# Kernel tuning notes

Measured on AMD Instinct MI355X. Metric: run time of the kernel, lower is better.

## Reference

```python
import jax, jax.numpy as jnp
import numpy as np

N = 32768      # nodes
E = 262144     # edges (avg degree 8)
F = 64         # channels per irrep
Z = 10         # species
R = 8          # radial basis size
H = 64         # radial MLP hidden
P_TP = 5       # TP paths: 0x0->0, 0x1->1, 1x0->1, 1x1->0, 1x1->1
P_SC = 9       # symmetric-contraction paths up to correlation 3
EPS = 0.25     # epsilon ~ 1/sqrt(avg_num_neighbors)


def _split(x):
    # [N, 4F] -> scalars [N,F], vectors [N,F,3] (irreps F x (0e + 1o))
    return x[:, :F], x[:, F:].reshape(x.shape[0], F, 3)


def _merge(s, v):
    return jnp.concatenate([s, v.reshape(v.shape[0], 3 * F)], axis=-1)


def _lin(s, v, Ws, Wv):
    # irreps-wise linear (separate channel mixing per l), fan-in normalized
    inv = 1.0 / np.sqrt(F)
    return (s @ Ws) * inv, jnp.einsum('nfc,fg->ngc', v, Wv) * inv


def _linZ(s, v, Ws, Wv, species):
    # per-species indexed linear, extra 1/sqrt(num_species) as in linZ
    inv = 1.0 / np.sqrt(F * Z)
    return (jnp.einsum('nf,nfg->ng', s, Ws[species]) * inv,
            jnp.einsum('nfc,nfg->ngc', v, Wv[species]) * inv)


def setup_inputs() -> dict:
    key = jax.random.key(0)
    ks = jax.random.split(key, 24)
    f32 = jnp.float32
    return {
        'vectors': jax.random.normal(ks[0], (E, 3), f32),
        'node_feats': jax.random.normal(ks[1], (N, 4 * F), f32),
        'radial_embeddings': jax.random.normal(ks[2], (E, R), f32),
        'W_skip_s': jax.random.normal(ks[3], (Z, F, F), f32),
        'W_skip_v': jax.random.normal(ks[4], (Z, F, F), f32),
        'W_up_s': jax.random.normal(ks[5], (F, F), f32),
        'W_up_v': jax.random.normal(ks[6], (F, F), f32),
        'W_mlp1': jax.random.normal(ks[7], (R, H), f32),
        'W_mlp2': jax.random.normal(ks[8], (H, H), f32),
        'W_mlp3': jax.random.normal(ks[9], (H, H), f32),
        'W_mlp4': jax.random.normal(ks[10], (H, P_TP * F), f32),
        'W_down_s': jax.random.normal(ks[11], (F, F), f32),
        'W_down_v': jax.random.normal(ks[12], (F, F), f32),
        'W_sc': jax.random.normal(ks[13], (Z, P_SC, F), f32),
        'W_post_s': jax.random.normal(ks[14], (F, F), f32),
        'W_post_v': jax.random.normal(ks[15], (F, F), f32),
        'W_out': jax.random.normal(ks[16], (F, 1), f32),
        'node_species': jax.random.randint(ks[17], (N,), 0, Z),
        'senders': jax.random.randint(ks[18], (E,), 0, N),
        'receivers': jax.random.randint(ks[19], (E,), 0, N),
    }


def reference(vectors, node_feats, radial_embeddings, W_skip_s, W_skip_v,
              W_up_s, W_up_v, W_mlp1, W_mlp2, W_mlp3, W_mlp4,
              W_down_s, W_down_v, W_sc, W_post_s, W_post_v, W_out,
              node_species, senders, receivers):
    s, v = _split(node_feats)

    # self connection: per-species skip linear (linZ_skip_tp)
    skip_s, skip_v = _linZ(s, v, W_skip_s, W_skip_v, node_species)

    # linear_up
    s, v = _lin(s, v, W_up_s, W_up_v)

    # spherical harmonics of edge vectors (l=0 is constant, l=1 = unit vector)
    Y1 = vectors / (jnp.linalg.norm(vectors, axis=-1, keepdims=True) + 1e-9)  # [E,3]

    # radial MLP (64,64,64,P_TP*F), no bias, fan-in normalized, silu
    act = jax.nn.silu
    h = act(radial_embeddings @ W_mlp1 * (1.0 / np.sqrt(R)))
    h = act(h @ W_mlp2 * (1.0 / np.sqrt(H)))
    h = act(h @ W_mlp3 * (1.0 / np.sqrt(H)))
    w = (h @ W_mlp4 * (1.0 / np.sqrt(H))).reshape(E, P_TP, F)  # per-edge path weights

    # channelwise tensor product: gather senders, CG-couple with Y, scatter to receivers
    ss = s[senders]              # [E,F]
    vv = v[senders]              # [E,F,3]
    dot = jnp.einsum('efc,ec->ef', vv, Y1)        # 1x1 -> 0
    cross = jnp.cross(vv, Y1[:, None, :])         # 1x1 -> 1
    m_s = w[:, 0] * ss + w[:, 3] * dot
    m_v = (w[:, 1][..., None] * Y1[:, None, :]
           + w[:, 2][..., None] * vv
           + w[:, 4][..., None] * cross * (1.0 / np.sqrt(2.0)))
    s = jax.ops.segment_sum(m_s * EPS, receivers, num_segments=N)  # [N,F]
    v = jax.ops.segment_sum(m_v * EPS, receivers, num_segments=N)  # [N,F,3]

    # linear_down
    s, v = _lin(s, v, W_down_s, W_down_v)

    # per-species symmetric contraction, correlation orders 1..3
    wz = W_sc[node_species]             # [N,P_SC,F]
    vn2 = jnp.sum(v * v, axis=-1)       # [N,F] invariant |v|^2
    s_out = (wz[:, 0] * s + wz[:, 1] * s * s + wz[:, 2] * vn2
             + wz[:, 3] * s ** 3 + wz[:, 4] * s * vn2)
    v_out = (wz[:, 5] + wz[:, 6] * s + wz[:, 7] * s * s + wz[:, 8] * vn2)[..., None] * v

    # linear_post_sc + skip connection
    s, v = _lin(s_out, v_out, W_post_s, W_post_v)
    s = s + skip_s
    v = v + skip_v

    # linear_readout to scalar output irreps (0e)
    node_outputs = s @ W_out * (1.0 / np.sqrt(F))  # [N,1]
    return node_outputs, _merge(s, v)
```

## Files before the change

kernel.cpp:

```cpp
#include <hip/hip_runtime.h>
#include <math.h>


#define NN 32768
#define EE 262144
#define EC 131072
#define ZZ 10
#define NB 128
#define NT_MAX 2064
#define INV8 0.125f
#define INV_SQRT8 0.35355339059327373f
#define INVZ 0.039528470752104741f
#define EPS_C 0.25f
#define RS2 0.70710678118654752f

typedef _Float16 f16;
typedef f16 f16x8 __attribute__((ext_vector_type(8)));
typedef f16 f16x4 __attribute__((ext_vector_type(4)));
typedef float f32x4 __attribute__((ext_vector_type(4)));

#define LDFRAG(fid) (*(const f16x8*)(fragw + ((size_t)(fid) << 9) + (lane << 3)))

__device__ __forceinline__ unsigned bfpair(float lo, float hi) {
  unsigned ul = __float_as_uint(lo);
  unsigned uh = __float_as_uint(hi);
  ul = (ul + 0x7FFFu + ((ul >> 16) & 1u)) >> 16;
  uh = (uh + 0x7FFFu + ((uh >> 16) & 1u)) >> 16;
  return ul | (uh << 16);
}

__device__ __forceinline__ unsigned short f2h(float x) {
  union { f16 h; unsigned short u; } cv;
  cv.h = (f16)x;
  return cv.u;
}

__device__ __forceinline__ f16x8 pack8(float4 a, float4 b) {
  f16x8 r;
  r[0] = (f16)a.x; r[1] = (f16)a.y; r[2] = (f16)a.z; r[3] = (f16)a.w;
  r[4] = (f16)b.x; r[5] = (f16)b.y; r[6] = (f16)b.z; r[7] = (f16)b.w;
  return r;
}

__device__ __forceinline__ float silu_f(float x) {
  return x / (1.0f + __expf(-x));
}

__global__ __launch_bounds__(256) void k_frag(
    const float* __restrict__ W1, const float* __restrict__ W2,
    const float* __restrict__ W3, const float* __restrict__ W4,
    const float* __restrict__ Wdns, const float* __restrict__ Wdnv,
    const float* __restrict__ Wpss, const float* __restrict__ Wpsv,
    const float* __restrict__ Wsks, const float* __restrict__ Wskv,
    const float* __restrict__ Wups, const float* __restrict__ Wupv,
    unsigned short* __restrict__ fragw) {
  int id = blockIdx.x * 256 + threadIdx.x;
  if (id >= 268 * 64) return;
  int fid = id >> 6, lane = id & 63;
  int q = lane >> 4, c = lane & 15;
  const float* W; int K = 64, N = 64, t, ks; float sc; int w4 = 0;
  if (fid < 4)       { W = W1; K = 8; N = 64; t = fid; ks = 0; sc = INV_SQRT8; }
  else if (fid < 12) { W = W2; t = (fid - 4) >> 1;  ks = (fid - 4) & 1;  sc = INV8; }
  else if (fid < 20) { W = W3; t = (fid - 12) >> 1; ks = (fid - 12) & 1; sc = INV8; }
  else if (fid < 60) { W = W4; N = 320; t = (fid - 20) >> 1; ks = (fid - 20) & 1; sc = INV8; w4 = 1; }
  else {
    int f2 = fid - 60; sc = INV8;
    if (f2 < 8)        { W = Wdns; }
    else if (f2 < 16)  { W = Wdnv; f2 -= 8; }
    else if (f2 < 24)  { W = Wpss; f2 -= 16; }
    else if (f2 < 32)  { W = Wpsv; f2 -= 24; }
    else if (f2 < 112) { f2 -= 32; W = Wsks + (f2 >> 3) * 4096; f2 &= 7; sc = INVZ; }
    else if (f2 < 192) { f2 -= 112; W = Wskv + (f2 >> 3) * 4096; f2 &= 7; sc = INVZ; }
    else if (f2 < 200) { W = Wups; f2 -= 192; }
    else               { W = Wupv; f2 -= 200; }
    t = f2 >> 1; ks = f2 & 1;
  }
  int col = w4 ? ((t % 5) * 64 + 4 * c + (t / 5)) : (t * 16 + c);
  unsigned short o[8];
#pragma unroll
  for (int i = 0; i < 8; ++i) {
    int k = ks * 32 + 8 * q + i;
    float v = (k < K) ? W[k * N + col] * sc : 0.0f;
    o[i] = f2h(v);
  }
  *(uint4*)(fragw + (size_t)id * 8) = *(const uint4*)o;
}

__global__ __launch_bounds__(256) void k_hist(const int* __restrict__ rcv,
                                              int* __restrict__ cnt) {
  int e = blockIdx.x * 256 + threadIdx.x;
  atomicAdd(&cnt[rcv[e]], 1);
}

__global__ __launch_bounds__(1024) void k_scan(const int* __restrict__ cnt,
                                               int* __restrict__ row_start,
                                               int* __restrict__ cursor) {
  __shared__ int tot[1024];
  int t = threadIdx.x;
  int base = t * 32;
  int local[32];
  int s = 0;
#pragma unroll
  for (int i = 0; i < 32; ++i) { local[i] = s; s += cnt[base + i]; }
  tot[t] = s;
  __syncthreads();
  for (int off = 1; off < 1024; off <<= 1) {
    int v = (t >= off) ? tot[t - off] : 0;
    __syncthreads();
    tot[t] += v;
    __syncthreads();
  }
  int prefix = (t == 0) ? 0 : tot[t - 1];
#pragma unroll
  for (int i = 0; i < 32; ++i) {
    int v = prefix + local[i];
    row_start[base + i] = v;
    cursor[base + i] = v;
  }
  if (t == 1023) row_start[NN] = prefix + s;
}

__global__ __launch_bounds__(256) void k_fill(const int* __restrict__ rcv,
                                              int* __restrict__ cursor,
                                              int* __restrict__ elist) {
  int e = blockIdx.x * 256 + threadIdx.x;
  int pos = atomicAdd(&cursor[rcv[e]], 1);
  elist[pos] = e;
}

__global__ __launch_bounds__(256) void k_nhist(const int* __restrict__ species,
                                               int* __restrict__ sbins,
                                               int* __restrict__ bcnt) {
  __shared__ int h[ZZ];
  int t = threadIdx.x;
  if (t < ZZ) h[t] = 0;
  __syncthreads();
  int n = blockIdx.x * 256 + t;
  atomicAdd(&h[species[n]], 1);
  __syncthreads();
  if (t < ZZ) {
    bcnt[blockIdx.x * ZZ + t] = h[t];
    atomicAdd(&sbins[32 + t], h[t]);
  }
}

__global__ __launch_bounds__(256) void k_nscan(int* __restrict__ sbins,
                                               const int* __restrict__ bcnt,
                                               int* __restrict__ bbase,
                                               int* __restrict__ tspec) {
  __shared__ int sb[12];
  int t = threadIdx.x;
  if (t == 0) {
    int off = 0;
    for (int z = 0; z < ZZ; ++z) {
      sb[z] = off;
      off += ((sbins[32 + z] + 15) >> 4) << 4;
    }
    sb[ZZ] = off;
  }
  __syncthreads();
  if (t < ZZ) {
    int run = sb[t];
    for (int b = 0; b < NB; ++b) {
      bbase[b * ZZ + t] = run;
      run += bcnt[b * ZZ + t];
    }
  }
  for (int i = t; i < NT_MAX; i += 256) {
    int base = i * 16, z = -1;
#pragma unroll
    for (int zz = 0; zz < ZZ; ++zz)
      if (base >= sb[zz] && base < sb[zz + 1]) z = zz;
    tspec[i] = z;
  }
}

__global__ __launch_bounds__(256) void k_nfill(const int* __restrict__ species,
                                               const int* __restrict__ bbase,
                                               int* __restrict__ nperm) {
  __shared__ int cur[ZZ];
  int t = threadIdx.x;
  if (t < ZZ) cur[t] = bbase[blockIdx.x * ZZ + t];
  __syncthreads();
  int n = blockIdx.x * 256 + t;
  int pos = atomicAdd(&cur[species[n]], 1);
  nperm[pos] = n;
}

__global__ __launch_bounds__(256) void k_up2(
    const float* __restrict__ nf,
    const unsigned short* __restrict__ fragw,
    unsigned short* __restrict__ s_up, unsigned short* __restrict__ v_up) {
  int lane = threadIdx.x & 63;
  int wv = threadIdx.x >> 6;
  int n0 = (blockIdx.x * 4 + wv) * 16;
  int q = lane >> 4, c = lane & 15;
  const f32x4 zero4 = {0.f, 0.f, 0.f, 0.f};
  const float* nrow = nf + (size_t)(n0 + c) * 256;

  f16x8 aS[2], aX[2], aY[2], aZ[2];
#pragma unroll
  for (int ks = 0; ks < 2; ++ks) {
    int k0 = ks * 32 + 8 * q;
    aS[ks] = pack8(*(const float4*)(nrow + k0), *(const float4*)(nrow + k0 + 4));
    float vb[24];
    const float4* vp = (const float4*)(nrow + 64 + 3 * k0);
#pragma unroll
    for (int j = 0; j < 6; ++j) *(float4*)(vb + 4 * j) = vp[j];
#pragma unroll
    for (int i = 0; i < 8; ++i) {
      aX[ks][i] = (f16)vb[3 * i];
      aY[ks][i] = (f16)vb[3 * i + 1];
      aZ[ks][i] = (f16)vb[3 * i + 2];
    }
  }

  f32x4 os[4], ox[4], oy[4], oz[4];
#pragma unroll
  for (int t = 0; t < 4; ++t)
#pragma unroll
    for (int ks = 0; ks < 2; ++ks) {
      f16x8 bS = LDFRAG(252 + t * 2 + ks);
      f16x8 bV = LDFRAG(260 + t * 2 + ks);
      os[t] = __builtin_amdgcn_mfma_f32_16x16x32_f16(aS[ks], bS, ks ? os[t] : zero4, 0, 0, 0);
      ox[t] = __builtin_amdgcn_mfma_f32_16x16x32_f16(aX[ks], bV, ks ? ox[t] : zero4, 0, 0, 0);
      oy[t] = __builtin_amdgcn_mfma_f32_16x16x32_f16(aY[ks], bV, ks ? oy[t] : zero4, 0, 0, 0);
      oz[t] = __builtin_amdgcn_mfma_f32_16x16x32_f16(aZ[ks], bV, ks ? oz[t] : zero4, 0, 0, 0);
    }

#pragma unroll
  for (int t = 0; t < 4; ++t)
#pragma unroll
    for (int r = 0; r < 4; ++r) {
      int n = n0 + 4 * q + r;
      int ch = 16 * t + c;
      s_up[n * 64 + ch] = f2h(os[t][r]);
      v_up[(n * 3 + 0) * 64 + ch] = f2h(ox[t][r]);
      v_up[(n * 3 + 1) * 64 + ch] = f2h(oy[t][r]);
      v_up[(n * 3 + 2) * 64 + ch] = f2h(oz[t][r]);
    }
}

__global__ __launch_bounds__(256) void k_mlp(
    const float* __restrict__ re, const int* __restrict__ elist,
    const float* __restrict__ vecs, const int* __restrict__ snd,
    const unsigned short* __restrict__ fragw,
    const unsigned short* __restrict__ s_up,
    const unsigned short* __restrict__ v_up,
    unsigned short* __restrict__ wm, int ip0) {
  __shared__ float hs[4][2][1088];
  int lane = threadIdx.x & 63;
  int wv = threadIdx.x >> 6;
  int q = lane >> 4, c = lane & 15;
  int ipb = ip0 + (blockIdx.x * 4 + wv) * 32;
  float* hw0 = hs[wv][0];
  float* hw1 = hs[wv][1];
  const f32x4 zero4 = {0.f, 0.f, 0.f, 0.f};

  f16x8 a1[2];
#pragma unroll
  for (int m = 0; m < 2; ++m) {
    f16x8 v = {0, 0, 0, 0, 0, 0, 0, 0};
    if (q == 0) {
      int e = elist[ipb + m * 16 + c];
      const float4* rp = (const float4*)(re + (size_t)e * 8);
      v = pack8(rp[0], rp[1]);
    }
    a1[m] = v;
  }
  {
    f32x4 acc[2][4];
#pragma unroll
    for (int t = 0; t < 4; ++t) {
      f16x8 b = LDFRAG(t);
#pragma unroll
      for (int m = 0; m < 2; ++m)
        acc[m][t] = __builtin_amdgcn_mfma_f32_16x16x32_f16(a1[m], b, zero4, 0, 0, 0);
    }
#pragma unroll
    for (int m = 0; m < 2; ++m) {
      float* hw = (m == 0) ? hw0 : hw1;
#pragma unroll
      for (int t = 0; t < 4; ++t)
#pragma unroll
        for (int r = 0; r < 4; ++r) {
          float x = silu_f(acc[m][t][r]);
          hw[(4 * q + r) * 68 + ((16 * t + c) ^ (r << 3))] = x;
        }
    }
  }

#pragma unroll
  for (int L = 0; L < 2; ++L) {
    int base = 4 + 8 * L;
    f16x8 af[2][2];
#pragma unroll
    for (int m = 0; m < 2; ++m) {
      const float* hw = (m == 0) ? hw0 : hw1;
#pragma unroll
      for (int ks = 0; ks < 2; ++ks) {
        const float* hp = hw + c * 68 + ks * 32 + 8 * (q ^ (c & 3));
        af[m][ks] = pack8(*(const float4*)hp, *(const float4*)(hp + 4));
      }
    }
    f32x4 acc[2][4];
#pragma unroll
    for (int t = 0; t < 4; ++t)
#pragma unroll
      for (int ks = 0; ks < 2; ++ks) {
        f16x8 b = LDFRAG(base + t * 2 + ks);
#pragma unroll
        for (int m = 0; m < 2; ++m)
          acc[m][t] = __builtin_amdgcn_mfma_f32_16x16x32_f16(
              af[m][ks], b, ks ? acc[m][t] : zero4, 0, 0, 0);
      }
#pragma unroll
    for (int m = 0; m < 2; ++m) {
      float* hw = (m == 0) ? hw0 : hw1;
#pragma unroll
      for (int t = 0; t < 4; ++t)
#pragma unroll
        for (int r = 0; r < 4; ++r) {
          float x = silu_f(acc[m][t][r]);
          hw[(4 * q + r) * 68 + ((16 * t + c) ^ (r << 3))] = x;
        }
    }
  }

  size_t orow = (size_t)(ipb - ip0);
#pragma unroll 1
  for (int m = 0; m < 2; ++m) {
    const float* hw = (m == 0) ? hw0 : hw1;
    f16x8 a4k0, a4k1;
    {
      const float* hp0 = hw + c * 68 + 8 * (q ^ (c & 3));
      const float* hp1 = hp0 + 32;
      a4k0 = pack8(*(const float4*)hp0, *(const float4*)(hp0 + 4));
      a4k1 = pack8(*(const float4*)hp1, *(const float4*)(hp1 + 4));
    }

    float Yx[4], Yy[4], Yz[4];
    f16x4 fs[4], fx[4], fy[4], fz[4];
#pragma unroll
    for (int r = 0; r < 4; ++r) {
      int e = elist[ipb + m * 16 + 4 * q + r];
      float ex = vecs[(size_t)e * 3 + 0];
      float ey = vecs[(size_t)e * 3 + 1];
      float ez = vecs[(size_t)e * 3 + 2];
      float rn = 1.0f / (sqrtf(ex * ex + ey * ey + ez * ez) + 1e-9f);
      Yx[r] = ex * rn; Yy[r] = ey * rn; Yz[r] = ez * rn;
      int se = snd[e];
      const unsigned short* sr = s_up + (size_t)se * 64 + 4 * c;
      const unsigned short* vr = v_up + (size_t)se * 192 + 4 * c;
      fs[r] = *(const f16x4*)sr;
      fx[r] = *(const f16x4*)vr;
      fy[r] = *(const f16x4*)(vr + 64);
      fz[r] = *(const f16x4*)(vr + 128);
    }

    float pms[4], pmx[4], pmy[4], pmz[4];
    unsigned k0s[4], k0x[4], k0y[4], k0z[4];
#pragma unroll
    for (int ig = 0; ig < 4; ++ig) {
      f32x4 o[5];
#pragma unroll
      for (int p = 0; p < 5; ++p) {
        f16x8 b0 = LDFRAG(20 + (ig * 5 + p) * 2 + 0);
        f16x8 b1 = LDFRAG(20 + (ig * 5 + p) * 2 + 1);
        o[p] = __builtin_amdgcn_mfma_f32_16x16x32_f16(a4k0, b0, zero4, 0, 0, 0);
        o[p] = __builtin_amdgcn_mfma_f32_16x16x32_f16(a4k1, b1, o[p], 0, 0, 0);
      }
#pragma unroll
      for (int r = 0; r < 4; ++r) {
        float ss = (float)fs[r][ig];
        float vx = (float)fx[r][ig], vy = (float)fy[r][ig], vz = (float)fz[r][ig];
        float dt = vx * Yx[r] + vy * Yy[r] + vz * Yz[r];
        float cx = vy * Yz[r] - vz * Yy[r];
        float cy = vz * Yx[r] - vx * Yz[r];
        float cz = vx * Yy[r] - vy * Yx[r];
        float ms = EPS_C * (o[0][r] * ss + o[3][r] * dt);
        float mx = EPS_C * (o[1][r] * Yx[r] + o[2][r] * vx + o[4][r] * (cx * RS2));
        float my = EPS_C * (o[1][r] * Yy[r] + o[2][r] * vy + o[4][r] * (cy * RS2));
        float mz = EPS_C * (o[1][r] * Yz[r] + o[2][r] * vz + o[4][r] * (cz * RS2));
        if (ig == 0) {
          pms[r] = ms; pmx[r] = mx; pmy[r] = my; pmz[r] = mz;
        } else if (ig == 1) {
          k0s[r] = bfpair(pms[r], ms); k0x[r] = bfpair(pmx[r], mx);
          k0y[r] = bfpair(pmy[r], my); k0z[r] = bfpair(pmz[r], mz);
        } else if (ig == 2) {
          pms[r] = ms; pmx[r] = mx; pmy[r] = my; pmz[r] = mz;
        } else {
          unsigned short* wr = wm + (orow + m * 16 + 4 * q + r) * 256 + 4 * c;
          uint2 v;
          v.x = k0s[r]; v.y = bfpair(pms[r], ms);
          *(uint2*)(wr) = v;
          v.x = k0x[r]; v.y = bfpair(pmx[r], mx);
          *(uint2*)(wr + 64) = v;
          v.x = k0y[r]; v.y = bfpair(pmy[r], my);
          *(uint2*)(wr + 128) = v;
          v.x = k0z[r]; v.y = bfpair(pmz[r], mz);
          *(uint2*)(wr + 192) = v;
        }
      }
    }
  }
}

__global__ __launch_bounds__(256) void k_gather(
    const unsigned short* __restrict__ m_buf,
    const int* __restrict__ row_start,
    float* __restrict__ acc, int e0, int e1) {
  int g = threadIdx.x & 63;
  int wv = threadIdx.x >> 6;
  int n = blockIdx.x * 4 + wv;
  int beg = row_start[n], end = row_start[n + 1];
  int lo = beg > e0 ? beg : e0;
  int hi = end < e1 ? end : e1;
  if (lo >= hi) return;
  float4 a = make_float4(0.f, 0.f, 0.f, 0.f);
  for (int i = lo; i < hi; ++i) {
    uint2 m = *(const uint2*)(m_buf + (size_t)(i - e0) * 256 + g * 4);
    a.x += __uint_as_float(m.x << 16);
    a.y += __uint_as_float(m.x & 0xFFFF0000u);
    a.z += __uint_as_float(m.y << 16);
    a.w += __uint_as_float(m.y & 0xFFFF0000u);
  }
  float* dst = acc + (size_t)n * 256 + g * 4;
  float4 p = *(const float4*)dst;
  *(float4*)dst = make_float4(a.x + p.x, a.y + p.y, a.z + p.z, a.w + p.w);
}

__global__ __launch_bounds__(128) void k_post2(
    const float* __restrict__ nf, const float* __restrict__ acc,
    const unsigned short* __restrict__ fragw,
    const float* __restrict__ Wsc, const float* __restrict__ Wout,
    const int* __restrict__ nperm, const int* __restrict__ tspec,
    float* __restrict__ out) {
  __shared__ float hs[2][2][1088];
  int lane = threadIdx.x & 63;
  int wv = threadIdx.x >> 6;
  int tt = blockIdx.x * 2 + wv;
  int spec = tspec[tt];
  if (spec < 0) return;
  int q = lane >> 4, c = lane & 15;
  float* hw0 = hs[wv][0];
  float* hw1 = hs[wv][1];
  const f32x4 zero4 = {0.f, 0.f, 0.f, 0.f};

  int nA = nperm[tt * 16 + c];
  size_t rowA = (size_t)((nA < 0) ? 0 : nA);
  const float* arow = acc + rowA * 256;
  const float* nrow = nf + rowA * 256;

  f16x8 aS[2], aVX[2], aVY[2], aVZ[2];
  f16x8 kS[2], kX[2], kY[2], kZ[2];
#pragma unroll
  for (int ks = 0; ks < 2; ++ks) {
    int k0 = ks * 32 + 8 * q;
    aS[ks]  = pack8(*(const float4*)(arow + k0),       *(const float4*)(arow + k0 + 4));
    aVX[ks] = pack8(*(const float4*)(arow + 64 + k0),  *(const float4*)(arow + 68 + k0));
    aVY[ks] = pack8(*(const float4*)(arow + 128 + k0), *(const float4*)(arow + 132 + k0));
    aVZ[ks] = pack8(*(const float4*)(arow + 192 + k0), *(const float4*)(arow + 196 + k0));
    kS[ks]  = pack8(*(const float4*)(nrow + k0),       *(const float4*)(nrow + k0 + 4));
    float vb[24];
    const float4* vp = (const float4*)(nrow + 64 + 3 * k0);
#pragma unroll
    for (int j = 0; j < 6; ++j) *(float4*)(vb + 4 * j) = vp[j];
#pragma unroll
    for (int i = 0; i < 8; ++i) {
      kX[ks][i] = (f16)vb[3 * i];
      kY[ks][i] = (f16)vb[3 * i + 1];
      kZ[ks][i] = (f16)vb[3 * i + 2];
    }
  }

  f32x4 ds[4], dvx[4], dvy[4], dvz[4];
#pragma unroll
  for (int t = 0; t < 4; ++t)
#pragma unroll
    for (int ks = 0; ks < 2; ++ks) {
      f16x8 bS = LDFRAG(60 + t * 2 + ks);
      f16x8 bV = LDFRAG(68 + t * 2 + ks);
      ds[t]  = __builtin_amdgcn_mfma_f32_16x16x32_f16(aS[ks],  bS, ks ? ds[t]  : zero4, 0, 0, 0);
      dvx[t] = __builtin_amdgcn_mfma_f32_16x16x32_f16(aVX[ks], bV, ks ? dvx[t] : zero4, 0, 0, 0);
      dvy[t] = __builtin_amdgcn_mfma_f32_16x16x32_f16(aVY[ks], bV, ks ? dvy[t] : zero4, 0, 0, 0);
      dvz[t] = __builtin_amdgcn_mfma_f32_16x16x32_f16(aVZ[ks], bV, ks ? dvz[t] : zero4, 0, 0, 0);
    }

  f32x4 ps[4], pvx[4], pvy[4], pvz[4];
#pragma unroll
  for (int t = 0; t < 4; ++t)
#pragma unroll
    for (int ks = 0; ks < 2; ++ks) {
      f16x8 bs = LDFRAG(92 + spec * 8 + t * 2 + ks);
      f16x8 bv = LDFRAG(172 + spec * 8 + t * 2 + ks);
      ps[t]  = __builtin_amdgcn_mfma_f32_16x16x32_f16(kS[ks], bs, ks ? ps[t]  : zero4, 0, 0, 0);
      pvx[t] = __builtin_amdgcn_mfma_f32_16x16x32_f16(kX[ks], bv, ks ? pvx[t] : zero4, 0, 0, 0);
      pvy[t] = __builtin_amdgcn_mfma_f32_16x16x32_f16(kY[ks], bv, ks ? pvy[t] : zero4, 0, 0, 0);
      pvz[t] = __builtin_amdgcn_mfma_f32_16x16x32_f16(kZ[ks], bv, ks ? pvz[t] : zero4, 0, 0, 0);
    }

  f32x4 so[4], vcm[4];
  const float* wzp = Wsc + spec * 576 + c;
#pragma unroll
  for (int t = 0; t < 4; ++t) {
    int col = 16 * t;
    float w0 = wzp[col], w1 = wzp[64 + col], w2 = wzp[128 + col];
    float w3 = wzp[192 + col], w4 = wzp[256 + col];
    float w5 = wzp[320 + col], w6 = wzp[384 + col];
    float w7 = wzp[448 + col], w8 = wzp[512 + col];
#pragma unroll
    for (int r = 0; r < 4; ++r) {
      float s = ds[t][r];
      float vx = dvx[t][r], vy = dvy[t][r], vz = dvz[t][r];
      float vn2 = vx * vx + vy * vy + vz * vz;
      so[t][r]  = w0 * s + w1 * s * s + w2 * vn2 + w3 * s * s * s + w4 * s * vn2;
      vcm[t][r] = w5 + w6 * s + w7 * s * s + w8 * vn2;
    }
  }

#pragma unroll
  for (int t = 0; t < 4; ++t)
#pragma unroll
    for (int r = 0; r < 4; ++r) {
      int ad = (4 * q + r) * 68 + ((16 * t + c) ^ (r << 3));
      hw0[ad] = so[t][r];
      hw1[ad] = vcm[t][r] * dvx[t][r];
    }
  {
    f16x8 aP0[2], aP1[2];
#pragma unroll
    for (int ks = 0; ks < 2; ++ks) {
      const float* hp0 = hw0 + c * 68 + ks * 32 + 8 * (q ^ (c & 3));
      const float* hp1 = hw1 + c * 68 + ks * 32 + 8 * (q ^ (c & 3));
      aP0[ks] = pack8(*(const float4*)hp0, *(const float4*)(hp0 + 4));
      aP1[ks] = pack8(*(const float4*)hp1, *(const float4*)(hp1 + 4));
    }
#pragma unroll
    for (int t = 0; t < 4; ++t)
#pragma unroll
      for (int ks = 0; ks < 2; ++ks) {
        ps[t]  = __builtin_amdgcn_mfma_f32_16x16x32_f16(aP0[ks], LDFRAG(76 + t * 2 + ks), ps[t], 0, 0, 0);
        pvx[t] = __builtin_amdgcn_mfma_f32_16x16x32_f16(aP1[ks], LDFRAG(84 + t * 2 + ks), pvx[t], 0, 0, 0);
      }
  }
#pragma unroll
  for (int t = 0; t < 4; ++t)
#pragma unroll
    for (int r = 0; r < 4; ++r) {
      int ad = (4 * q + r) * 68 + ((16 * t + c) ^ (r << 3));
      hw0[ad] = vcm[t][r] * dvy[t][r];
      hw1[ad] = vcm[t][r] * dvz[t][r];
    }
  {
    f16x8 aP0[2], aP1[2];
#pragma unroll
    for (int ks = 0; ks < 2; ++ks) {
      const float* hp0 = hw0 + c * 68 + ks * 32 + 8 * (q ^ (c & 3));
      const float* hp1 = hw1 + c * 68 + ks * 32 + 8 * (q ^ (c & 3));
      aP0[ks] = pack8(*(const float4*)hp0, *(const float4*)(hp0 + 4));
      aP1[ks] = pack8(*(const float4*)hp1, *(const float4*)(hp1 + 4));
    }
#pragma unroll
    for (int t = 0; t < 4; ++t)
#pragma unroll
      for (int ks = 0; ks < 2; ++ks) {
        pvy[t] = __builtin_amdgcn_mfma_f32_16x16x32_f16(aP0[ks], LDFRAG(84 + t * 2 + ks), pvy[t], 0, 0, 0);
        pvz[t] = __builtin_amdgcn_mfma_f32_16x16x32_f16(aP1[ks], LDFRAG(84 + t * 2 + ks), pvz[t], 0, 0, 0);
      }
  }

  float wo[4];
#pragma unroll
  for (int t = 0; t < 4; ++t) wo[t] = Wout[16 * t + c];
  int nst[4];
#pragma unroll
  for (int r = 0; r < 4; ++r) nst[r] = nperm[tt * 16 + 4 * q + r];
#pragma unroll
  for (int r = 0; r < 4; ++r) {
    float part = 0.f;
#pragma unroll
    for (int t = 0; t < 4; ++t) part += ps[t][r] * wo[t];
    part += __shfl_xor(part, 1);
    part += __shfl_xor(part, 2);
    part += __shfl_xor(part, 4);
    part += __shfl_xor(part, 8);
    int n = nst[r];
    if (n >= 0) {
      float* orow = out + NN + (size_t)n * 256;
#pragma unroll
      for (int t = 0; t < 4; ++t) {
        int col = 16 * t + c;
        orow[col] = ps[t][r];
        orow[64 + col * 3 + 0] = pvx[t][r];
        orow[64 + col * 3 + 1] = pvy[t][r];
        orow[64 + col * 3 + 2] = pvz[t][r];
      }
      if (c == 0) out[n] = part * INV8;
    }
  }
}

extern "C" void kernel_launch(void* const* d_in, const int* in_sizes, int n_in,
                              void* d_out, int out_size, void* d_ws, size_t ws_size,
                              hipStream_t stream) {
  (void)in_sizes; (void)n_in; (void)out_size; (void)ws_size;
  const float* vecs = (const float*)d_in[0];
  const float* nf   = (const float*)d_in[1];
  const float* re   = (const float*)d_in[2];
  const float* Wsks = (const float*)d_in[3];
  const float* Wskv = (const float*)d_in[4];
  const float* Wups = (const float*)d_in[5];
  const float* Wupv = (const float*)d_in[6];
  const float* W1   = (const float*)d_in[7];
  const float* W2   = (const float*)d_in[8];
  const float* W3   = (const float*)d_in[9];
  const float* W4   = (const float*)d_in[10];
  const float* Wdns = (const float*)d_in[11];
  const float* Wdnv = (const float*)d_in[12];
  const float* Wsc  = (const float*)d_in[13];
  const float* Wpss = (const float*)d_in[14];
  const float* Wpsv = (const float*)d_in[15];
  const float* Wout = (const float*)d_in[16];
  const int* species = (const int*)d_in[17];
  const int* snd     = (const int*)d_in[18];
  const int* rcv     = (const int*)d_in[19];

  float* ws = (float*)d_ws;
  unsigned short* s_up  = (unsigned short*)ws;
  unsigned short* v_up  = (unsigned short*)(ws + 1048576);
  float* acc   = ws + 4194304;
  unsigned short* fragw = (unsigned short*)(ws + 12582912);
  int* row_st  = (int*)(ws + 12651520);
  int* cursor  = (int*)(ws + 12684352);
  int* elist   = (int*)(ws + 12717120);
  int* nperm   = (int*)(ws + 12979264);
  int* tspec   = (int*)(ws + 13012544);
  int* sbins   = (int*)(ws + 13014848);
  int* bcnt    = (int*)(ws + 13014912);
  int* bbase   = (int*)(ws + 13016192);
  unsigned short* wm = (unsigned short*)(ws + 13017472);

  hipMemsetAsync(cursor, 0, NN * sizeof(int), stream);
  hipMemsetAsync(acc, 0, (size_t)NN * 256 * sizeof(float), stream);
  hipMemsetAsync(sbins, 0, 64 * sizeof(int), stream);
  hipMemsetAsync(nperm, 0xFF, NT_MAX * 16 * sizeof(int), stream);
  k_frag<<<67, 256, 0, stream>>>(W1, W2, W3, W4, Wdns, Wdnv, Wpss, Wpsv,
                                 Wsks, Wskv, Wups, Wupv, fragw);
  k_hist<<<EE / 256, 256, 0, stream>>>(rcv, cursor);
  k_scan<<<1, 1024, 0, stream>>>(cursor, row_st, cursor);
  k_fill<<<EE / 256, 256, 0, stream>>>(rcv, cursor, elist);
  k_nhist<<<NB, 256, 0, stream>>>(species, sbins, bcnt);
  k_nscan<<<1, 256, 0, stream>>>(sbins, bcnt, bbase, tspec);
  k_nfill<<<NB, 256, 0, stream>>>(species, bbase, nperm);
  k_up2<<<512, 256, 0, stream>>>(nf, fragw, s_up, v_up);
  for (int c = 0; c < 2; ++c) {
    k_mlp<<<EC / 128, 256, 0, stream>>>(re, elist, vecs, snd, fragw,
                                        s_up, v_up, wm, c * EC);
    k_gather<<<NN / 4, 256, 0, stream>>>(wm, row_st, acc, c * EC, (c + 1) * EC);
  }
  k_post2<<<NT_MAX / 2, 128, 0, stream>>>(nf, acc, fragw, Wsc, Wout,
                                          nperm, tspec, (float*)d_out);
}
```

Baseline: 408.9 us.

## Halve per-wave edge tile in k_mlp and split gather into two channel passes

Each wave in the edge MLP kernel now handles 16 edges instead of 32. The block count doubles and shared memory per wave halves. The sender-feature gather and message write are split into two passes over channel pairs, which lowers live registers, and launch bounds request 4 blocks per SM for higher occupancy. The cost is less reuse of each weight fragment load across edges, narrower global loads and stores (4-byte instead of 8-byte), and a second pass that repeats the gather addressing.

New measurement: 377.6 us. -7.6%, faster.

```diff
diff --git a/kernel.cpp b/kernel.cpp
--- a/kernel.cpp
+++ b/kernel.cpp
@@ -17,6 +17,7 @@
 typedef _Float16 f16;
 typedef f16 f16x8 __attribute__((ext_vector_type(8)));
 typedef f16 f16x4 __attribute__((ext_vector_type(4)));
+typedef f16 f16x2 __attribute__((ext_vector_type(2)));
 typedef float f32x4 __attribute__((ext_vector_type(4)));
 
 #define LDFRAG(fid) (*(const f16x8*)(fragw + ((size_t)(fid) << 9) + (lane << 3)))
@@ -241,139 +242,114 @@
     }
 }
 
-__global__ __launch_bounds__(256) void k_mlp(
+__global__ __launch_bounds__(256, 4) void k_mlp(
     const float* __restrict__ re, const int* __restrict__ elist,
     const float* __restrict__ vecs, const int* __restrict__ snd,
     const unsigned short* __restrict__ fragw,
     const unsigned short* __restrict__ s_up,
     const unsigned short* __restrict__ v_up,
     unsigned short* __restrict__ wm, int ip0) {
-  __shared__ float hs[4][2][1088];
+  __shared__ float hs[4][1088];
   int lane = threadIdx.x & 63;
   int wv = threadIdx.x >> 6;
   int q = lane >> 4, c = lane & 15;
-  int ipb = ip0 + (blockIdx.x * 4 + wv) * 32;
-  float* hw0 = hs[wv][0];
-  float* hw1 = hs[wv][1];
+  int ipb = ip0 + (blockIdx.x * 4 + wv) * 16;
+  float* hw = hs[wv];
   const f32x4 zero4 = {0.f, 0.f, 0.f, 0.f};
 
-  f16x8 a1[2];
-#pragma unroll
-  for (int m = 0; m < 2; ++m) {
-    f16x8 v = {0, 0, 0, 0, 0, 0, 0, 0};
-    if (q == 0) {
-      int e = elist[ipb + m * 16 + c];
-      const float4* rp = (const float4*)(re + (size_t)e * 8);
-      v = pack8(rp[0], rp[1]);
-    }
-    a1[m] = v;
+  f16x8 a1 = {0, 0, 0, 0, 0, 0, 0, 0};
+  if (q == 0) {
+    int e = elist[ipb + c];
+    const float4* rp = (const float4*)(re + (size_t)e * 8);
+    a1 = pack8(rp[0], rp[1]);
   }
   {
-    f32x4 acc[2][4];
-#pragma unroll
-    for (int t = 0; t < 4; ++t) {
-      f16x8 b = LDFRAG(t);
-#pragma unroll
-      for (int m = 0; m < 2; ++m)
-        acc[m][t] = __builtin_amdgcn_mfma_f32_16x16x32_f16(a1[m], b, zero4, 0, 0, 0);
-    }
-#pragma unroll
-    for (int m = 0; m < 2; ++m) {
-      float* hw = (m == 0) ? hw0 : hw1;
-#pragma unroll
-      for (int t = 0; t < 4; ++t)
-#pragma unroll
-        for (int r = 0; r < 4; ++r) {
-          float x = silu_f(acc[m][t][r]);
-          hw[(4 * q + r) * 68 + ((16 * t + c) ^ (r << 3))] = x;
-        }
-    }
+    f32x4 acc[4];
+#pragma unroll
+    for (int t = 0; t < 4; ++t)
+      acc[t] = __builtin_amdgcn_mfma_f32_16x16x32_f16(a1, LDFRAG(t), zero4, 0, 0, 0);
+#pragma unroll
+    for (int t = 0; t < 4; ++t)
+#pragma unroll
+      for (int r = 0; r < 4; ++r) {
+        float x = silu_f(acc[t][r]);
+        hw[(4 * q + r) * 68 + ((16 * t + c) ^ (r << 3))] = x;
+      }
   }
 
 #pragma unroll
   for (int L = 0; L < 2; ++L) {
     int base = 4 + 8 * L;
-    f16x8 af[2][2];
-#pragma unroll
-    for (int m = 0; m < 2; ++m) {
-      const float* hw = (m == 0) ? hw0 : hw1;
-#pragma unroll
-      for (int ks = 0; ks < 2; ++ks) {
-        const float* hp = hw + c * 68 + ks * 32 + 8 * (q ^ (c & 3));
-        af[m][ks] = pack8(*(const float4*)hp, *(const float4*)(hp + 4));
+    f16x8 af0, af1;
+    {
+      const float* hp = hw + c * 68 + 8 * (q ^ (c & 3));
+      af0 = pack8(*(const float4*)hp, *(const float4*)(hp + 4));
+      af1 = pack8(*(const float4*)(hp + 32), *(const float4*)(hp + 36));
+    }
+    f32x4 acc[4];
+#pragma unroll
+    for (int t = 0; t < 4; ++t) {
+      acc[t] = __builtin_amdgcn_mfma_f32_16x16x32_f16(af0, LDFRAG(base + t * 2), zero4, 0, 0, 0);
+      acc[t] = __builtin_amdgcn_mfma_f32_16x16x32_f16(af1, LDFRAG(base + t * 2 + 1), acc[t], 0, 0, 0);
+    }
+#pragma unroll
+    for (int t = 0; t < 4; ++t)
+#pragma unroll
+      for (int r = 0; r < 4; ++r) {
+        float x = silu_f(acc[t][r]);
+        hw[(4 * q + r) * 68 + ((16 * t + c) ^ (r << 3))] = x;
       }
-    }
-    f32x4 acc[2][4];
-#pragma unroll
-    for (int t = 0; t < 4; ++t)
-#pragma unroll
-      for (int ks = 0; ks < 2; ++ks) {
-        f16x8 b = LDFRAG(base + t * 2 + ks);
-#pragma unroll
-        for (int m = 0; m < 2; ++m)
-          acc[m][t] = __builtin_amdgcn_mfma_f32_16x16x32_f16(
-              af[m][ks], b, ks ? acc[m][t] : zero4, 0, 0, 0);
-      }
-#pragma unroll
-    for (int m = 0; m < 2; ++m) {
-      float* hw = (m == 0) ? hw0 : hw1;
-#pragma unroll
-      for (int t = 0; t < 4; ++t)
-#pragma unroll
-        for (int r = 0; r < 4; ++r) {
-          float x = silu_f(acc[m][t][r]);
-          hw[(4 * q + r) * 68 + ((16 * t + c) ^ (r << 3))] = x;
-        }
-    }
+  }
+
+  f16x8 a4k0, a4k1;
+  {
+    const float* hp = hw + c * 68 + 8 * (q ^ (c & 3));
+    a4k0 = pack8(*(const float4*)hp, *(const float4*)(hp + 4));
+    a4k1 = pack8(*(const float4*)(hp + 32), *(const float4*)(hp + 36));
+  }
+
+  int se_[4];
+  float Yx[4], Yy[4], Yz[4];
+#pragma unroll
+  for (int r = 0; r < 4; ++r) {
+    int e = elist[ipb + 4 * q + r];
+    float ex = vecs[(size_t)e * 3 + 0];
+    float ey = vecs[(size_t)e * 3 + 1];
+    float ez = vecs[(size_t)e * 3 + 2];
+    float rn = 1.0f / (sqrtf(ex * ex + ey * ey + ez * ez) + 1e-9f);
+    Yx[r] = ex * rn; Yy[r] = ey * rn; Yz[r] = ez * rn;
+    se_[r] = snd[e];
   }
 
   size_t orow = (size_t)(ipb - ip0);
 #pragma unroll 1
-  for (int m = 0; m < 2; ++m) {
-    const float* hw = (m == 0) ? hw0 : hw1;
-    f16x8 a4k0, a4k1;
-    {
-      const float* hp0 = hw + c * 68 + 8 * (q ^ (c & 3));
-      const float* hp1 = hp0 + 32;
-      a4k0 = pack8(*(const float4*)hp0, *(const float4*)(hp0 + 4));
-      a4k1 = pack8(*(const float4*)hp1, *(const float4*)(hp1 + 4));
-    }
-
-    float Yx[4], Yy[4], Yz[4];
-    f16x4 fs[4], fx[4], fy[4], fz[4];
+  for (int pg = 0; pg < 2; ++pg) {
+    f16x2 gs[4], gx[4], gy[4], gz[4];
 #pragma unroll
     for (int r = 0; r < 4; ++r) {
-      int e = elist[ipb + m * 16 + 4 * q + r];
-      float ex = vecs[(size_t)e * 3 + 0];
-      float ey = vecs[(size_t)e * 3 + 1];
-      float ez = vecs[(size_t)e * 3 + 2];
-      float rn = 1.0f / (sqrtf(ex * ex + ey * ey + ez * ez) + 1e-9f);
-      Yx[r] = ex * rn; Yy[r] = ey * rn; Yz[r] = ez * rn;
-      int se = snd[e];
-      const unsigned short* sr = s_up + (size_t)se * 64 + 4 * c;
-      const unsigned short* vr = v_up + (size_t)se * 192 + 4 * c;
-      fs[r] = *(const f16x4*)sr;
-      fx[r] = *(const f16x4*)vr;
-      fy[r] = *(const f16x4*)(vr + 64);
-      fz[r] = *(const f16x4*)(vr + 128);
-    }
-
+      const unsigned short* sr = s_up + (size_t)se_[r] * 64 + 4 * c + 2 * pg;
+      const unsigned short* vr = v_up + (size_t)se_[r] * 192 + 4 * c + 2 * pg;
+      gs[r] = *(const f16x2*)sr;
+      gx[r] = *(const f16x2*)vr;
+      gy[r] = *(const f16x2*)(vr + 64);
+      gz[r] = *(const f16x2*)(vr + 128);
+    }
     float pms[4], pmx[4], pmy[4], pmz[4];
-    unsigned k0s[4], k0x[4], k0y[4], k0z[4];
-#pragma unroll
-    for (int ig = 0; ig < 4; ++ig) {
+#pragma unroll
+    for (int ig2 = 0; ig2 < 2; ++ig2) {
+      int ig = 2 * pg + ig2;
       f32x4 o[5];
 #pragma unroll
       for (int p = 0; p < 5; ++p) {
-        f16x8 b0 = LDFRAG(20 + (ig * 5 + p) * 2 + 0);
-        f16x8 b1 = LDFRAG(20 + (ig * 5 + p) * 2 + 1);
-        o[p] = __builtin_amdgcn_mfma_f32_16x16x32_f16(a4k0, b0, zero4, 0, 0, 0);
-        o[p] = __builtin_amdgcn_mfma_f32_16x16x32_f16(a4k1, b1, o[p], 0, 0, 0);
+        o[p] = __builtin_amdgcn_mfma_f32_16x16x32_f16(
+            a4k0, LDFRAG(20 + (ig * 5 + p) * 2 + 0), zero4, 0, 0, 0);
+        o[p] = __builtin_amdgcn_mfma_f32_16x16x32_f16(
+            a4k1, LDFRAG(20 + (ig * 5 + p) * 2 + 1), o[p], 0, 0, 0);
       }
 #pragma unroll
       for (int r = 0; r < 4; ++r) {
-        float ss = (float)fs[r][ig];
-        float vx = (float)fx[r][ig], vy = (float)fy[r][ig], vz = (float)fz[r][ig];
+        float ss = (float)gs[r][ig2];
+        float vx = (float)gx[r][ig2], vy = (float)gy[r][ig2], vz = (float)gz[r][ig2];
         float dt = vx * Yx[r] + vy * Yy[r] + vz * Yz[r];
         float cx = vy * Yz[r] - vz * Yy[r];
         float cy = vz * Yx[r] - vx * Yz[r];
@@ -382,24 +358,14 @@
         float mx = EPS_C * (o[1][r] * Yx[r] + o[2][r] * vx + o[4][r] * (cx * RS2));
         float my = EPS_C * (o[1][r] * Yy[r] + o[2][r] * vy + o[4][r] * (cy * RS2));
         float mz = EPS_C * (o[1][r] * Yz[r] + o[2][r] * vz + o[4][r] * (cz * RS2));
-        if (ig == 0) {
-          pms[r] = ms; pmx[r] = mx; pmy[r] = my; pmz[r] = mz;
-        } else if (ig == 1) {
-          k0s[r] = bfpair(pms[r], ms); k0x[r] = bfpair(pmx[r], mx);
-          k0y[r] = bfpair(pmy[r], my); k0z[r] = bfpair(pmz[r], mz);
-        } else if (ig == 2) {
+        if (ig2 == 0) {
           pms[r] = ms; pmx[r] = mx; pmy[r] = my; pmz[r] = mz;
         } else {
-          unsigned short* wr = wm + (orow + m * 16 + 4 * q + r) * 256 + 4 * c;
-          uint2 v;
-          v.x = k0s[r]; v.y = bfpair(pms[r], ms);
-          *(uint2*)(wr) = v;
-          v.x = k0x[r]; v.y = bfpair(pmx[r], mx);
-          *(uint2*)(wr + 64) = v;
-          v.x = k0y[r]; v.y = bfpair(pmy[r], my);
-          *(uint2*)(wr + 128) = v;
-          v.x = k0z[r]; v.y = bfpair(pmz[r], mz);
-          *(uint2*)(wr + 192) = v;
+          unsigned short* wr = wm + (orow + 4 * q + r) * 256 + 4 * c + 2 * pg;
+          *(unsigned*)(wr)       = bfpair(pms[r], ms);
+          *(unsigned*)(wr + 64)  = bfpair(pmx[r], mx);
+          *(unsigned*)(wr + 128) = bfpair(pmy[r], my);
+          *(unsigned*)(wr + 192) = bfpair(pmz[r], mz);
         }
       }
     }
@@ -655,8 +621,8 @@
   k_nfill<<<NB, 256, 0, stream>>>(species, bbase, nperm);
   k_up2<<<512, 256, 0, stream>>>(nf, fragw, s_up, v_up);
   for (int c = 0; c < 2; ++c) {
-    k_mlp<<<EC / 128, 256, 0, stream>>>(re, elist, vecs, snd, fragw,
-                                        s_up, v_up, wm, c * EC);
+    k_mlp<<<EC / 64, 256, 0, stream>>>(re, elist, vecs, snd, fragw,
+                                       s_up, v_up, wm, c * EC);
     k_gather<<<NN / 4, 256, 0, stream>>>(wm, row_st, acc, c * EC, (c + 1) * EC);
   }
   k_post2<<<NT_MAX / 2, 128, 0, stream>>>(nf, acc, fragw, Wsc, Wout,
```
